# Kernel tuning notes

Measured on AMD Instinct MI355X. Metric: run time of the kernel, lower is better.

Reference implementation:

```python
import jax, jax.numpy as jnp
import numpy as np

N_HEAD, D_MODEL, D_K, D_V = 16, 1024, 64, 64
BIAS_WEIGHT = 1.0
NEG = -10000.0


def setup_inputs() -> dict:
    key = jax.random.key(0)
    ks = jax.random.split(key, 9)
    B, L = 2, 2048
    q = jax.random.normal(ks[0], (B, L, D_MODEL), dtype=jnp.float32)
    k = jax.random.normal(ks[1], (B, L, D_MODEL), dtype=jnp.float32)
    v = jax.random.normal(ks[2], (B, L, D_MODEL), dtype=jnp.float32)
    mask = jax.random.randint(ks[3], (B, L, L), 0, 2, dtype=jnp.int32)
    bias = jax.random.normal(ks[4], (B, L, L), dtype=jnp.float32)
    s = 1.0 / np.sqrt(D_MODEL)
    w_qs = jax.random.uniform(ks[5], (D_MODEL, N_HEAD * D_K), jnp.float32, -s, s)
    w_ks = jax.random.uniform(ks[6], (D_MODEL, N_HEAD * D_K), jnp.float32, -s, s)
    w_vs = jax.random.uniform(ks[7], (D_MODEL, N_HEAD * D_V), jnp.float32, -s, s)
    w_fc = jax.random.uniform(ks[8], (N_HEAD * D_V, D_MODEL), jnp.float32, -s, s)
    return {"q": q, "k": k, "v": v, "mask": mask, "bias": bias,
            "w_qs": w_qs, "w_ks": w_ks, "w_vs": w_vs, "w_fc": w_fc}


def reference(q, k, v, mask, bias, w_qs, w_ks, w_vs, w_fc):
    B, Lq, _ = q.shape
    # project and split heads: [B, H, L, d]
    qh = (q @ w_qs).reshape(B, Lq, N_HEAD, D_K).transpose(0, 2, 1, 3)
    kh = (k @ w_ks).reshape(B, k.shape[1], N_HEAD, D_K).transpose(0, 2, 1, 3)
    vh = (v @ w_vs).reshape(B, v.shape[1], N_HEAD, D_V).transpose(0, 2, 1, 3)
    temperature = D_K ** 0.5
    attn = jnp.einsum('bhqd,bhkd->bhqk', qh / temperature, kh)
    attn = attn + bias[:, None, :, :] * BIAS_WEIGHT
    attn = jnp.where(mask[:, None, :, :] == 0, NEG, attn)
    attn = jax.nn.softmax(attn, axis=-1)
    out = jnp.einsum('bhqk,bhkd->bhqd', attn, vh)
    out = out.transpose(0, 2, 1, 3).reshape(B, Lq, N_HEAD * D_V)
    return out @ w_fc
```

## Files before the change

### kernel.cpp

```cpp
#include <hip/hip_runtime.h>
#include <cstddef>

#define DEV static __device__ __forceinline__

typedef float f32x4 __attribute__((ext_vector_type(4)));
typedef __bf16 bf16x8 __attribute__((ext_vector_type(8)));
typedef __bf16 bf16x4v __attribute__((ext_vector_type(4)));
typedef unsigned short u16x8 __attribute__((ext_vector_type(8)));
typedef unsigned short u16x4 __attribute__((ext_vector_type(4)));
typedef unsigned u32x2 __attribute__((ext_vector_type(2)));
typedef unsigned u32x4 __attribute__((ext_vector_type(4)));
typedef _Float16 f16;
typedef _Float16 f16x4 __attribute__((ext_vector_type(4)));

constexpr int BB = 2, LL = 2048, DM = 1024, NH = 16, DK = 64;
constexpr float LOG2E = 1.44269504f;

DEV unsigned short f2bf(float f) {
  unsigned u = __builtin_bit_cast(unsigned, f);
  u += 0x7fffu + ((u >> 16) & 1u);
  return (unsigned short)(u >> 16);
}
DEV u16x4 cvt4(f32x4 v) {
  bf16x4v b = __builtin_convertvector(v, bf16x4v);
  return __builtin_bit_cast(u16x4, b);
}
DEV bf16x8 asbf(u16x8 v) { return __builtin_bit_cast(bf16x8, v); }
DEV f32x4 mfma16(u16x8 a, u16x8 b, f32x4 c) {
  return __builtin_amdgcn_mfma_f32_16x16x32_bf16(asbf(a), asbf(b), c, 0, 0, 0);
}
#if __has_builtin(__builtin_amdgcn_exp2f)
DEV float fexp2(float x) { return __builtin_amdgcn_exp2f(x); }
#else
DEV float fexp2(float x) { return exp2f(x); }
#endif
DEV void swap32(unsigned& a, unsigned& b) {
#if __has_builtin(__builtin_amdgcn_permlane32_swap)
  u32x2 r = __builtin_amdgcn_permlane32_swap(a, b, false, false);
  a = r[0]; b = r[1];
#else
  asm("v_permlane32_swap_b32 %0, %1" : "+v"(a), "+v"(b));
#endif
}
DEV void swap16(unsigned& a, unsigned& b) {
#if __has_builtin(__builtin_amdgcn_permlane16_swap)
  u32x2 r = __builtin_amdgcn_permlane16_swap(a, b, false, false);
  a = r[0]; b = r[1];
#else
  asm("v_permlane16_swap_b32 %0, %1" : "+v"(a), "+v"(b));
#endif
}
DEV void g2lds16(const void* g, void* l) {
  __builtin_amdgcn_global_load_lds(
      (const __attribute__((address_space(1))) unsigned int*)g,
      (__attribute__((address_space(3))) unsigned int*)l, 16, 0, 0);
}

__global__ __launch_bounds__(256) void prep_all(
    const float* __restrict__ w0, const float* __restrict__ w1,
    const float* __restrict__ w2, const float* __restrict__ w3,
    unsigned short* __restrict__ wT, const int* __restrict__ mask,
    const float* __restrict__ bias, f16* __restrict__ bmf,
    const float* __restrict__ s0, const float* __restrict__ s1,
    const float* __restrict__ s2, unsigned short* __restrict__ qkvb) {
  int f = blockIdx.x, t = threadIdx.x;
  if (f < 4096) {
    __shared__ float tile[32][33];
    int z = f >> 10, rem = f & 1023;
    int k0 = (rem >> 5) * 32, n0 = (rem & 31) * 32;
    const float* W = (z == 0) ? w0 : (z == 1) ? w1 : (z == 2) ? w2 : w3;
    unsigned short* out = wT + (size_t)z * DM * DM;
    int tx = t & 31, ty = t >> 5;
#pragma unroll
    for (int p = 0; p < 4; p++)
      tile[ty + 8 * p][tx] = W[(size_t)(k0 + ty + 8 * p) * DM + n0 + tx];
    __syncthreads();
#pragma unroll
    for (int p = 0; p < 4; p++)
      out[(size_t)(n0 + ty + 8 * p) * DM + k0 + tx] = f2bf(tile[tx][ty + 8 * p]);
  } else if (f < 12288) {
    int f2 = f - 4096;
    int w = t >> 6, lane = t & 63;
    int bq = f2 >> 5;
    int kt = (f2 & 31) * 4 + w;
    int b = bq >> 7, qt = bq & 127;
    int q = qt * 16 + (lane & 15);
    int k = kt * 16 + (lane >> 4) * 4;
    size_t src = ((size_t)b * LL + q) * LL + k;
    int4 mk = *(const int4*)(mask + src);
    float4 bs = *(const float4*)(bias + src);
    f16x4 o;
    o[0] = (f16)((mk.x == 0 ? -10000.f : bs.x) * LOG2E);
    o[1] = (f16)((mk.y == 0 ? -10000.f : bs.y) * LOG2E);
    o[2] = (f16)((mk.z == 0 ? -10000.f : bs.z) * LOG2E);
    o[3] = (f16)((mk.w == 0 ? -10000.f : bs.w) * LOG2E);
    *(f16x4*)(bmf + ((size_t)bq * 128 + kt) * 256 + lane * 4) = o;
  } else {
    int f3 = f - 12288;
    int z = f3 >> 11;
    const float* src = (z == 0) ? s0 : (z == 1) ? s1 : s2;
    size_t i = ((size_t)(f3 & 2047) * 256 + t) * 8;
    float4 a = *(const float4*)(src + i);
    float4 b = *(const float4*)(src + i + 4);
    u16x8 o;
    o[0] = f2bf(a.x); o[1] = f2bf(a.y); o[2] = f2bf(a.z); o[3] = f2bf(a.w);
    o[4] = f2bf(b.x); o[5] = f2bf(b.y); o[6] = f2bf(b.z); o[7] = f2bf(b.w);
    *(u16x8*)(qkvb + (size_t)z * (size_t)(BB * LL) * DM + i) = o;
  }
}

template <int KITERS>
DEV void gemm_core(const unsigned short* __restrict__ A,
                   const unsigned short* __restrict__ BT,
                   unsigned short* Al, unsigned short* Bl,
                   int m0, int n0, int k0beg, int t, f32x4 (&acc)[4][4]) {
  int lane = t & 63, c = lane & 15, qd = lane >> 4;
  int w = t >> 6, wm = w >> 1, wn = w & 1;
  int r0 = t >> 3;
  int gsw = (t & 7) ^ (r0 & 7);

#pragma unroll 1
  for (int kk = 0; kk < KITERS; ++kk) {
    int k0 = k0beg + kk * 64;
#pragma unroll
    for (int p = 0; p < 4; ++p) {
      g2lds16(&A[(size_t)(m0 + 32 * p + r0) * DM + k0 + 8 * gsw],
              &Al[p * 2048 + w * 512]);
      g2lds16(&BT[(size_t)(n0 + 32 * p + r0) * DM + k0 + 8 * gsw],
              &Bl[p * 2048 + w * 512]);
    }
    __syncthreads();
#pragma unroll
    for (int ks = 0; ks < 2; ++ks) {
      u16x8 af[4], bfr[4];
#pragma unroll
      for (int mt = 0; mt < 4; ++mt)
        af[mt] = *(const u16x8*)&Al[(64 * wm + 16 * mt + c) * 64 +
                                    (((4 * ks + qd) ^ (c & 7)) << 3)];
#pragma unroll
      for (int nt = 0; nt < 4; ++nt)
        bfr[nt] = *(const u16x8*)&Bl[(64 * wn + 16 * nt + c) * 64 +
                                     (((4 * ks + qd) ^ (c & 7)) << 3)];
#pragma unroll
      for (int mt = 0; mt < 4; ++mt)
#pragma unroll
        for (int nt = 0; nt < 4; ++nt)
          acc[mt][nt] = mfma16(af[mt], bfr[nt], acc[mt][nt]);
    }
    __syncthreads();
  }
}

__global__ __launch_bounds__(256, 3) void proj_gemm(
    const unsigned short* __restrict__ qkvb, const unsigned short* __restrict__ wT,
    unsigned short* __restrict__ qh, unsigned short* __restrict__ kh,
    unsigned short* __restrict__ vT) {
  __shared__ unsigned short Al[128 * 64];
  __shared__ unsigned short Bl[128 * 64];
  int o = blockIdx.x;
  int wg = (o & 7) * 96 + (o >> 3);
  int z = wg >> 8, rem = wg & 255;
  int m0 = (rem >> 3) * 128, n0 = (rem & 7) * 128;
  const unsigned short* A = qkvb + (size_t)z * BB * LL * DM;
  const unsigned short* BT = wT + (size_t)z * DM * DM;
  int t = threadIdx.x, lane = t & 63, c = lane & 15, qd = lane >> 4;
  int w = t >> 6, wm = w >> 1, wn = w & 1;
  f32x4 acc[4][4] = {};
  gemm_core<DM / 64>(A, BT, Al, Bl, m0, n0, 0, t, acc);

  if (z == 2) {
#pragma unroll
    for (int mt = 0; mt < 4; ++mt)
#pragma unroll
      for (int nt = 0; nt < 4; ++nt) {
        int n = n0 + 64 * wn + 16 * nt + c;
        int h = n >> 6, d = n & 63;
        int m = m0 + 64 * wm + 16 * mt + 4 * qd;
        int b = m >> 11, l = m & 2047;
        *(u16x4*)&vT[(((size_t)b * NH + h) * DK + d) * LL + l] = cvt4(acc[mt][nt]);
      }
  } else {
    unsigned short* Ch = z ? kh : qh;
    float scale = z ? 1.0f : 0.125f * LOG2E;
#pragma unroll
    for (int mt = 0; mt < 4; ++mt)
#pragma unroll
      for (int nt = 0; nt < 4; ++nt) {
        int n = n0 + 64 * wn + 16 * nt + c;
        int h = n >> 6, d = n & 63;
#pragma unroll
        for (int i = 0; i < 4; ++i) {
          int m = m0 + 64 * wm + 16 * mt + 4 * qd + i;
          int b = m >> 11, l = m & 2047;
          Ch[(((size_t)b * NH + h) * LL + l) * DK + d] = f2bf(acc[mt][nt][i] * scale);
        }
      }
  }
}

__global__ __launch_bounds__(256, 3) void fc_gemm(const unsigned short* __restrict__ A,
                                                  const unsigned short* __restrict__ BT,
                                                  float* __restrict__ C) {
  __shared__ unsigned short Al[128 * 64];
  __shared__ unsigned short Bl[128 * 64];
  int o = blockIdx.x;
  int wg = (o & 7) * 32 + (o >> 3);
  int m0 = (wg >> 3) * 128, n0 = (wg & 7) * 128;
  int t = threadIdx.x, lane = t & 63, c = lane & 15, qd = lane >> 4;
  int w = t >> 6, wm = w >> 1, wn = w & 1;
  f32x4 acc[4][4] = {};
  gemm_core<DM / 64>(A, BT, Al, Bl, m0, n0, 0, t, acc);
#pragma unroll
  for (int mt = 0; mt < 4; ++mt)
#pragma unroll
    for (int nt = 0; nt < 4; ++nt) {
      int n = n0 + 64 * wn + 16 * nt + c;
#pragma unroll
      for (int i = 0; i < 4; ++i) {
        int m = m0 + 64 * wm + 16 * mt + 4 * qd + i;
        C[(size_t)m * DM + n] = acc[mt][nt][i];
      }
    }
}

__global__ __launch_bounds__(256, 4) void attn_kern(
    const unsigned short* __restrict__ qh, const unsigned short* __restrict__ kh,
    const unsigned short* __restrict__ vT, const f16* __restrict__ bmf,
    unsigned short* __restrict__ O) {
  __shared__ unsigned short Kb[2][4096];
  __shared__ unsigned short Vb[2][4096];

  int t = threadIdx.x, w = t >> 6, lane = t & 63, c = lane & 15, qd = lane >> 4;
  int q0 = blockIdx.x * 64, h = blockIdx.y, b = blockIdx.z;
  const unsigned short* Q = qh + (((size_t)b * NH + h) * LL + q0) * DK;
  const unsigned short* K = kh + ((size_t)b * NH + h) * LL * DK;
  const unsigned short* V = vT + ((size_t)b * NH + h) * DK * LL;
  const f16* BMF = bmf + (((size_t)b * 128 + blockIdx.x * 4 + w) * 128) * 256 +
                   lane * 4;
  int rt = t >> 3, gg = t & 7;

#pragma unroll
  for (int r = 0; r < 2; ++r) {
    int row = r * 32 + rt;
    int sc = ((gg ^ (row & 7)) << 3);
    g2lds16(&Q[(size_t)row * DK + sc], &Kb[1][r * 2048 + w * 512]);
    g2lds16(&K[(size_t)row * DK + sc], &Kb[0][r * 2048 + w * 512]);
    g2lds16(&V[(size_t)row * LL + sc], &Vb[0][r * 2048 + w * 512]);
  }
  f16x4 bA[4], bB[4];
#pragma unroll
  for (int mt = 0; mt < 4; ++mt) bA[mt] = *(const f16x4*)&BMF[(size_t)mt * 256];
  __syncthreads();

  u16x8 qf[2];
#pragma unroll
  for (int ks = 0; ks < 2; ++ks)
    qf[ks] = *(const u16x8*)&Kb[1][(16 * w + c) * 64 +
                                   (((4 * ks + qd) ^ (c & 7)) << 3)];
  __syncthreads();

  const u16x8 ones = {0x3F80, 0x3F80, 0x3F80, 0x3F80,
                      0x3F80, 0x3F80, 0x3F80, 0x3F80};
  f32x4 lacc = {};
  f32x4 oacc[4] = {};

  auto body = [&](int it, f16x4 (&bc)[4], f16x4 (&bn)[4]) {
    int cur = it & 1;
    const unsigned short* Kl = Kb[cur];
    const unsigned short* Vt = Vb[cur];
    if (it + 1 < 32) {
      int nb = cur ^ 1, kt1 = (it + 1) * 64;
#pragma unroll
      for (int r = 0; r < 2; ++r) {
        int row = r * 32 + rt;
        int sc = ((gg ^ (row & 7)) << 3);
        g2lds16(&K[(size_t)(kt1 + row) * DK + sc], &Kb[nb][r * 2048 + w * 512]);
        g2lds16(&V[(size_t)row * LL + kt1 + sc], &Vb[nb][r * 2048 + w * 512]);
      }
#pragma unroll
      for (int mt = 0; mt < 4; ++mt)
        bn[mt] = *(const f16x4*)&BMF[(size_t)((it + 1) * 4 + mt) * 256];
    }

    f32x4 s[4];
    __builtin_amdgcn_s_setprio(1);
#pragma unroll
    for (int mt = 0; mt < 4; ++mt) {
      int row = 16 * mt + c;
      u16x8 k0f = *(const u16x8*)&Kl[row * 64 + ((qd ^ (c & 7)) << 3)];
      u16x8 k1f = *(const u16x8*)&Kl[row * 64 + (((4 + qd) ^ (c & 7)) << 3)];
      f16x4 b4 = bc[mt];
      f32x4 z = {(float)b4[0], (float)b4[1], (float)b4[2], (float)b4[3]};
      z = mfma16(k0f, qf[0], z);
      s[mt] = mfma16(k1f, qf[1], z);
    }
    __builtin_amdgcn_s_setprio(0);
    u16x8 pf[2];
    {
      unsigned L[4], H[4];
#pragma unroll
      for (int mt = 0; mt < 4; ++mt) {
        f32x4 p;
#pragma unroll
        for (int i = 0; i < 4; ++i) p[i] = fexp2(s[mt][i]);
        u32x2 lw = __builtin_bit_cast(u32x2, cvt4(p));
        L[mt] = lw[0];
        H[mt] = lw[1];
      }
#pragma unroll
      for (int ks = 0; ks < 2; ++ks) {
        unsigned l0 = L[2 * ks], l1 = L[2 * ks + 1];
        unsigned h0 = H[2 * ks], h1 = H[2 * ks + 1];
        swap32(l0, l1); swap16(l0, l1);
        swap32(h0, h1); swap16(h0, h1);
        u32x4 pw = {l0, h0, l1, h1};
        pf[ks] = __builtin_bit_cast(u16x8, pw);
      }
    }
    __builtin_amdgcn_s_setprio(1);
    lacc = mfma16(ones, pf[0], lacc);
    lacc = mfma16(ones, pf[1], lacc);
#pragma unroll
    for (int dt = 0; dt < 4; ++dt) {
      int row = 16 * dt + c;
      u16x8 v0f = *(const u16x8*)&Vt[row * 64 + ((qd ^ (c & 7)) << 3)];
      u16x8 v1f = *(const u16x8*)&Vt[row * 64 + (((4 + qd) ^ (c & 7)) << 3)];
      oacc[dt] = mfma16(v0f, pf[0], oacc[dt]);
      oacc[dt] = mfma16(v1f, pf[1], oacc[dt]);
    }
    __builtin_amdgcn_s_setprio(0);
    __syncthreads();
  };

#pragma unroll 1
  for (int it = 0; it < 32; it += 2) {
    body(it, bA, bB);
    body(it + 1, bB, bA);
  }

  {
    float rl = 1.f / lacc[0];
    size_t orow = ((size_t)b * LL + q0 + 16 * w + c) * DM + h * DK;
#pragma unroll
    for (int dt = 0; dt < 4; ++dt)
      *(u16x4*)&O[orow + 16 * dt + 4 * qd] = cvt4(oacc[dt] * rl);
  }
}

extern "C" void kernel_launch(void* const* d_in, const int* in_sizes, int n_in,
                              void* d_out, int out_size, void* d_ws, size_t ws_size,
                              hipStream_t stream) {
  (void)in_sizes; (void)n_in; (void)ws_size; (void)out_size;
  const float* q = (const float*)d_in[0];
  const float* k = (const float*)d_in[1];
  const float* v = (const float*)d_in[2];
  const int* mask = (const int*)d_in[3];
  const float* bias = (const float*)d_in[4];
  const float* w_qs = (const float*)d_in[5];
  const float* w_ks = (const float*)d_in[6];
  const float* w_vs = (const float*)d_in[7];
  const float* w_fc = (const float*)d_in[8];

  char* ws = (char*)d_ws;
  const size_t MB = 1024 * 1024;
  unsigned short* wT = (unsigned short*)(ws);
  f16* bmf = (f16*)(ws + 8 * MB);
  unsigned short* qkvb = (unsigned short*)(ws + 24 * MB);
  unsigned short* qh = (unsigned short*)(ws + 48 * MB);
  unsigned short* kh = (unsigned short*)(ws + 56 * MB);
  unsigned short* vhT = (unsigned short*)(ws + 64 * MB);
  unsigned short* Obuf = (unsigned short*)(ws + 72 * MB);

  prep_all<<<dim3(18432), dim3(256), 0, stream>>>(w_qs, w_ks, w_vs, w_fc, wT,
                                                  mask, bias, bmf, q, k, v, qkvb);
  proj_gemm<<<dim3(768), 256, 0, stream>>>(qkvb, wT, qh, kh, vhT);
  attn_kern<<<dim3(32, 16, 2), 256, 0, stream>>>(qh, kh, vhT, bmf, Obuf);
  fc_gemm<<<dim3(256), 256, 0, stream>>>(Obuf, wT + (size_t)3 * DM * DM,
                                         (float*)d_out);
}
```

Baseline: 267.5 us.

## Use two-wave attention blocks with each wave handling 32 query rows

The attention kernel moves from 4 waves of 16 query rows each to 2 waves of 32 query rows each. Each K/V fragment read from LDS now feeds twice as many MFMAs, cutting LDS read traffic per unit of work. The launch is flattened to a 1D grid with a block-index swizzle that groups nearby work onto the same XCD, which should improve L2 reuse of K/V. The costs are more registers per wave (doubled accumulators and bias buffers), fewer waves per block to hide latency, and a lower launch-bounds occupancy hint.

Result: no change. 270.9 us (+1.2%).

```diff
diff --git a/kernel.cpp b/kernel.cpp
--- a/kernel.cpp
+++ b/kernel.cpp
@@ -223,7 +223,7 @@
     }
 }
 
-__global__ __launch_bounds__(256, 4) void attn_kern(
+__global__ __launch_bounds__(128, 2) void attn_kern(
     const unsigned short* __restrict__ qh, const unsigned short* __restrict__ kh,
     const unsigned short* __restrict__ vT, const f16* __restrict__ bmf,
     unsigned short* __restrict__ O) {
@@ -231,78 +231,93 @@
   __shared__ unsigned short Vb[2][4096];
 
   int t = threadIdx.x, w = t >> 6, lane = t & 63, c = lane & 15, qd = lane >> 4;
-  int q0 = blockIdx.x * 64, h = blockIdx.y, b = blockIdx.z;
+  int o = blockIdx.x;
+  int wg = (o & 7) * 128 + (o >> 3);
+  int x = wg & 31, h = (wg >> 5) & 15, b = wg >> 9;
+  int q0 = x * 64;
   const unsigned short* Q = qh + (((size_t)b * NH + h) * LL + q0) * DK;
   const unsigned short* K = kh + ((size_t)b * NH + h) * LL * DK;
   const unsigned short* V = vT + ((size_t)b * NH + h) * DK * LL;
-  const f16* BMF = bmf + (((size_t)b * 128 + blockIdx.x * 4 + w) * 128) * 256 +
-                   lane * 4;
+  const f16* BMF0 = bmf + (((size_t)b * 128 + x * 4 + 2 * w) * 128) * 256 + lane * 4;
+  const f16* BMF1 = BMF0 + (size_t)128 * 256;
   int rt = t >> 3, gg = t & 7;
 
 #pragma unroll
-  for (int r = 0; r < 2; ++r) {
-    int row = r * 32 + rt;
+  for (int r = 0; r < 4; ++r) {
+    int row = r * 16 + rt;
     int sc = ((gg ^ (row & 7)) << 3);
-    g2lds16(&Q[(size_t)row * DK + sc], &Kb[1][r * 2048 + w * 512]);
-    g2lds16(&K[(size_t)row * DK + sc], &Kb[0][r * 2048 + w * 512]);
-    g2lds16(&V[(size_t)row * LL + sc], &Vb[0][r * 2048 + w * 512]);
-  }
-  f16x4 bA[4], bB[4];
-#pragma unroll
-  for (int mt = 0; mt < 4; ++mt) bA[mt] = *(const f16x4*)&BMF[(size_t)mt * 256];
+    g2lds16(&Q[(size_t)row * DK + sc], &Kb[1][r * 1024 + w * 512]);
+    g2lds16(&K[(size_t)row * DK + sc], &Kb[0][r * 1024 + w * 512]);
+    g2lds16(&V[(size_t)row * LL + sc], &Vb[0][r * 1024 + w * 512]);
+  }
+  f16x4 bA[8], bB[8];
+#pragma unroll
+  for (int nt = 0; nt < 2; ++nt)
+#pragma unroll
+    for (int mt = 0; mt < 4; ++mt)
+      bA[nt * 4 + mt] = *(const f16x4*)((nt ? BMF1 : BMF0) + (size_t)mt * 256);
   __syncthreads();
 
-  u16x8 qf[2];
-#pragma unroll
-  for (int ks = 0; ks < 2; ++ks)
-    qf[ks] = *(const u16x8*)&Kb[1][(16 * w + c) * 64 +
-                                   (((4 * ks + qd) ^ (c & 7)) << 3)];
+  u16x8 qf[2][2];
+#pragma unroll
+  for (int nt = 0; nt < 2; ++nt)
+#pragma unroll
+    for (int ks = 0; ks < 2; ++ks)
+      qf[nt][ks] = *(const u16x8*)&Kb[1][(32 * w + 16 * nt + c) * 64 +
+                                         (((4 * ks + qd) ^ (c & 7)) << 3)];
   __syncthreads();
 
   const u16x8 ones = {0x3F80, 0x3F80, 0x3F80, 0x3F80,
                       0x3F80, 0x3F80, 0x3F80, 0x3F80};
-  f32x4 lacc = {};
-  f32x4 oacc[4] = {};
-
-  auto body = [&](int it, f16x4 (&bc)[4], f16x4 (&bn)[4]) {
+  f32x4 lacc[2] = {};
+  f32x4 oacc[4][2] = {};
+
+  auto body = [&](int it, f16x4 (&bc)[8], f16x4 (&bn)[8]) {
     int cur = it & 1;
     const unsigned short* Kl = Kb[cur];
     const unsigned short* Vt = Vb[cur];
     if (it + 1 < 32) {
       int nb = cur ^ 1, kt1 = (it + 1) * 64;
 #pragma unroll
-      for (int r = 0; r < 2; ++r) {
-        int row = r * 32 + rt;
+      for (int r = 0; r < 4; ++r) {
+        int row = r * 16 + rt;
         int sc = ((gg ^ (row & 7)) << 3);
-        g2lds16(&K[(size_t)(kt1 + row) * DK + sc], &Kb[nb][r * 2048 + w * 512]);
-        g2lds16(&V[(size_t)row * LL + kt1 + sc], &Vb[nb][r * 2048 + w * 512]);
-      }
-#pragma unroll
-      for (int mt = 0; mt < 4; ++mt)
-        bn[mt] = *(const f16x4*)&BMF[(size_t)((it + 1) * 4 + mt) * 256];
-    }
-
-    f32x4 s[4];
+        g2lds16(&K[(size_t)(kt1 + row) * DK + sc], &Kb[nb][r * 1024 + w * 512]);
+        g2lds16(&V[(size_t)row * LL + kt1 + sc], &Vb[nb][r * 1024 + w * 512]);
+      }
+#pragma unroll
+      for (int nt = 0; nt < 2; ++nt)
+#pragma unroll
+        for (int mt = 0; mt < 4; ++mt)
+          bn[nt * 4 + mt] = *(const f16x4*)((nt ? BMF1 : BMF0) +
+                                            (size_t)((it + 1) * 4 + mt) * 256);
+    }
+
+    f32x4 s[4][2];
     __builtin_amdgcn_s_setprio(1);
 #pragma unroll
     for (int mt = 0; mt < 4; ++mt) {
       int row = 16 * mt + c;
       u16x8 k0f = *(const u16x8*)&Kl[row * 64 + ((qd ^ (c & 7)) << 3)];
       u16x8 k1f = *(const u16x8*)&Kl[row * 64 + (((4 + qd) ^ (c & 7)) << 3)];
-      f16x4 b4 = bc[mt];
-      f32x4 z = {(float)b4[0], (float)b4[1], (float)b4[2], (float)b4[3]};
-      z = mfma16(k0f, qf[0], z);
-      s[mt] = mfma16(k1f, qf[1], z);
+#pragma unroll
+      for (int nt = 0; nt < 2; ++nt) {
+        f16x4 b4 = bc[nt * 4 + mt];
+        f32x4 z = {(float)b4[0], (float)b4[1], (float)b4[2], (float)b4[3]};
+        z = mfma16(k0f, qf[nt][0], z);
+        s[mt][nt] = mfma16(k1f, qf[nt][1], z);
+      }
     }
     __builtin_amdgcn_s_setprio(0);
-    u16x8 pf[2];
-    {
+    u16x8 pf[2][2];
+#pragma unroll
+    for (int nt = 0; nt < 2; ++nt) {
       unsigned L[4], H[4];
 #pragma unroll
       for (int mt = 0; mt < 4; ++mt) {
         f32x4 p;
 #pragma unroll
-        for (int i = 0; i < 4; ++i) p[i] = fexp2(s[mt][i]);
+        for (int i = 0; i < 4; ++i) p[i] = fexp2(s[mt][nt][i]);
         u32x2 lw = __builtin_bit_cast(u32x2, cvt4(p));
         L[mt] = lw[0];
         H[mt] = lw[1];
@@ -314,19 +329,25 @@
         swap32(l0, l1); swap16(l0, l1);
         swap32(h0, h1); swap16(h0, h1);
         u32x4 pw = {l0, h0, l1, h1};
-        pf[ks] = __builtin_bit_cast(u16x8, pw);
+        pf[nt][ks] = __builtin_bit_cast(u16x8, pw);
       }
     }
     __builtin_amdgcn_s_setprio(1);
-    lacc = mfma16(ones, pf[0], lacc);
-    lacc = mfma16(ones, pf[1], lacc);
+#pragma unroll
+    for (int nt = 0; nt < 2; ++nt) {
+      lacc[nt] = mfma16(ones, pf[nt][0], lacc[nt]);
+      lacc[nt] = mfma16(ones, pf[nt][1], lacc[nt]);
+    }
 #pragma unroll
     for (int dt = 0; dt < 4; ++dt) {
       int row = 16 * dt + c;
       u16x8 v0f = *(const u16x8*)&Vt[row * 64 + ((qd ^ (c & 7)) << 3)];
       u16x8 v1f = *(const u16x8*)&Vt[row * 64 + (((4 + qd) ^ (c & 7)) << 3)];
-      oacc[dt] = mfma16(v0f, pf[0], oacc[dt]);
-      oacc[dt] = mfma16(v1f, pf[1], oacc[dt]);
+#pragma unroll
+      for (int nt = 0; nt < 2; ++nt) {
+        oacc[dt][nt] = mfma16(v0f, pf[nt][0], oacc[dt][nt]);
+        oacc[dt][nt] = mfma16(v1f, pf[nt][1], oacc[dt][nt]);
+      }
     }
     __builtin_amdgcn_s_setprio(0);
     __syncthreads();
@@ -338,12 +359,13 @@
     body(it + 1, bB, bA);
   }
 
-  {
-    float rl = 1.f / lacc[0];
-    size_t orow = ((size_t)b * LL + q0 + 16 * w + c) * DM + h * DK;
+#pragma unroll
+  for (int nt = 0; nt < 2; ++nt) {
+    float rl = 1.f / lacc[nt][0];
+    size_t orow = ((size_t)b * LL + q0 + 32 * w + 16 * nt + c) * DM + h * DK;
 #pragma unroll
     for (int dt = 0; dt < 4; ++dt)
-      *(u16x4*)&O[orow + 16 * dt + 4 * qd] = cvt4(oacc[dt] * rl);
+      *(u16x4*)&O[orow + 16 * dt + 4 * qd] = cvt4(oacc[dt][nt] * rl);
   }
 }
 
@@ -374,7 +396,7 @@
   prep_all<<<dim3(18432), dim3(256), 0, stream>>>(w_qs, w_ks, w_vs, w_fc, wT,
                                                   mask, bias, bmf, q, k, v, qkvb);
   proj_gemm<<<dim3(768), 256, 0, stream>>>(qkvb, wT, qh, kh, vhT);
-  attn_kern<<<dim3(32, 16, 2), 256, 0, stream>>>(qh, kh, vhT, bmf, Obuf);
+  attn_kern<<<dim3(1024), dim3(128), 0, stream>>>(qh, kh, vhT, bmf, Obuf);
   fc_gemm<<<dim3(256), 256, 0, stream>>>(Obuf, wT + (size_t)3 * DM * DM,
                                          (float*)d_out);
 }
```

## Double-buffer fc_gemm LDS tiles and remap attention blocks across XCDs

Applied to the files above, without the earlier changes.

The output projection GEMM replaces the shared gemm_core call with an inline double-buffered loop that prefetches the next K-tile into a second LDS buffer while MFMAs run on the current one. This hides global-to-LDS latency at the cost of doubling LDS use and lowering the occupancy hint from 3 to 2 blocks per CU. The attention kernel switches to a 1D grid with a swizzled block index, so that consecutive blocks on the same XCD share a head's K/V and bias data for better L2 reuse.

Result: slower. 276.3 us (+3.3%).

```diff
diff --git a/kernel.cpp b/kernel.cpp
--- a/kernel.cpp
+++ b/kernel.cpp
@@ -198,18 +198,58 @@
   }
 }
 
-__global__ __launch_bounds__(256, 3) void fc_gemm(const unsigned short* __restrict__ A,
+__global__ __launch_bounds__(256, 2) void fc_gemm(const unsigned short* __restrict__ A,
                                                   const unsigned short* __restrict__ BT,
                                                   float* __restrict__ C) {
-  __shared__ unsigned short Al[128 * 64];
-  __shared__ unsigned short Bl[128 * 64];
+  __shared__ unsigned short Al[2][128 * 64];
+  __shared__ unsigned short Bl[2][128 * 64];
   int o = blockIdx.x;
   int wg = (o & 7) * 32 + (o >> 3);
   int m0 = (wg >> 3) * 128, n0 = (wg & 7) * 128;
   int t = threadIdx.x, lane = t & 63, c = lane & 15, qd = lane >> 4;
   int w = t >> 6, wm = w >> 1, wn = w & 1;
+  int r0 = t >> 3, gsw = (t & 7) ^ (r0 & 7);
   f32x4 acc[4][4] = {};
-  gemm_core<DM / 64>(A, BT, Al, Bl, m0, n0, 0, t, acc);
+
+  auto stage = [&](int kk, int buf) {
+    int k0 = kk * 64;
+#pragma unroll
+    for (int p = 0; p < 4; ++p) {
+      g2lds16(&A[(size_t)(m0 + 32 * p + r0) * DM + k0 + 8 * gsw],
+              &Al[buf][p * 2048 + w * 512]);
+      g2lds16(&BT[(size_t)(n0 + 32 * p + r0) * DM + k0 + 8 * gsw],
+              &Bl[buf][p * 2048 + w * 512]);
+    }
+  };
+  auto compute = [&](int buf) {
+#pragma unroll
+    for (int ks = 0; ks < 2; ++ks) {
+      u16x8 af[4], bfr[4];
+#pragma unroll
+      for (int mt = 0; mt < 4; ++mt)
+        af[mt] = *(const u16x8*)&Al[buf][(64 * wm + 16 * mt + c) * 64 +
+                                         (((4 * ks + qd) ^ (c & 7)) << 3)];
+#pragma unroll
+      for (int nt = 0; nt < 4; ++nt)
+        bfr[nt] = *(const u16x8*)&Bl[buf][(64 * wn + 16 * nt + c) * 64 +
+                                          (((4 * ks + qd) ^ (c & 7)) << 3)];
+#pragma unroll
+      for (int mt = 0; mt < 4; ++mt)
+#pragma unroll
+        for (int nt = 0; nt < 4; ++nt)
+          acc[mt][nt] = mfma16(af[mt], bfr[nt], acc[mt][nt]);
+    }
+  };
+
+  stage(0, 0);
+  __syncthreads();
+#pragma unroll 1
+  for (int kk = 0; kk < 16; ++kk) {
+    if (kk + 1 < 16) stage(kk + 1, (kk + 1) & 1);
+    compute(kk & 1);
+    __syncthreads();
+  }
+
 #pragma unroll
   for (int mt = 0; mt < 4; ++mt)
 #pragma unroll
@@ -231,12 +271,14 @@
   __shared__ unsigned short Vb[2][4096];
 
   int t = threadIdx.x, w = t >> 6, lane = t & 63, c = lane & 15, qd = lane >> 4;
-  int q0 = blockIdx.x * 64, h = blockIdx.y, b = blockIdx.z;
+  int o = blockIdx.x;
+  int wg = (o & 7) * 128 + (o >> 3);
+  int x = wg & 31, h = (wg >> 5) & 15, b = wg >> 9;
+  int q0 = x * 64;
   const unsigned short* Q = qh + (((size_t)b * NH + h) * LL + q0) * DK;
   const unsigned short* K = kh + ((size_t)b * NH + h) * LL * DK;
   const unsigned short* V = vT + ((size_t)b * NH + h) * DK * LL;
-  const f16* BMF = bmf + (((size_t)b * 128 + blockIdx.x * 4 + w) * 128) * 256 +
-                   lane * 4;
+  const f16* BMF = bmf + (((size_t)b * 128 + x * 4 + w) * 128) * 256 + lane * 4;
   int rt = t >> 3, gg = t & 7;
 
 #pragma unroll
@@ -374,7 +416,7 @@
   prep_all<<<dim3(18432), dim3(256), 0, stream>>>(w_qs, w_ks, w_vs, w_fc, wT,
                                                   mask, bias, bmf, q, k, v, qkvb);
   proj_gemm<<<dim3(768), 256, 0, stream>>>(qkvb, wT, qh, kh, vhT);
-  attn_kern<<<dim3(32, 16, 2), 256, 0, stream>>>(qh, kh, vhT, bmf, Obuf);
+  attn_kern<<<dim3(1024), dim3(256), 0, stream>>>(qh, kh, vhT, bmf, Obuf);
   fc_gemm<<<dim3(256), 256, 0, stream>>>(Obuf, wT + (size_t)3 * DM * DM,
                                          (float*)d_out);
 }
```

## Software-pipeline attention: overlap next QK^T MFMA with current softmax and PV

Applied to the files above, without the earlier changes.

Restructures the attention loop so the QK^T scores for the next key tile are computed while the current tile's exp/convert and PV MFMAs run, using a triple-buffered V in LDS and a prologue/epilogue. It also flattens the grid to 1D and remaps block indices so each group of 8 consecutive blocks is spread across different (batch, head, query) positions, aiming for better XCD/L2 locality. The intent is to hide MFMA and transcendental latency by interleaving them, at the cost of more LDS (an extra V buffer) and higher register pressure from keeping two score sets live.

New measurement: 267.1 us. No clear change (-0.1%).

```diff
diff --git a/kernel.cpp b/kernel.cpp
--- a/kernel.cpp
+++ b/kernel.cpp
@@ -228,17 +228,20 @@
     const unsigned short* __restrict__ vT, const f16* __restrict__ bmf,
     unsigned short* __restrict__ O) {
   __shared__ unsigned short Kb[2][4096];
-  __shared__ unsigned short Vb[2][4096];
+  __shared__ unsigned short Vb[3][4096];
 
   int t = threadIdx.x, w = t >> 6, lane = t & 63, c = lane & 15, qd = lane >> 4;
-  int q0 = blockIdx.x * 64, h = blockIdx.y, b = blockIdx.z;
+  int o = blockIdx.x;
+  int wg = (o & 7) * 128 + (o >> 3);
+  int x = wg & 31, h = (wg >> 5) & 15, b = wg >> 9;
+  int q0 = x * 64;
   const unsigned short* Q = qh + (((size_t)b * NH + h) * LL + q0) * DK;
   const unsigned short* K = kh + ((size_t)b * NH + h) * LL * DK;
   const unsigned short* V = vT + ((size_t)b * NH + h) * DK * LL;
-  const f16* BMF = bmf + (((size_t)b * 128 + blockIdx.x * 4 + w) * 128) * 256 +
-                   lane * 4;
+  const f16* BMF = bmf + (((size_t)b * 128 + x * 4 + w) * 128) * 256 + lane * 4;
   int rt = t >> 3, gg = t & 7;
 
+  f16x4 bc[4], bn[4];
 #pragma unroll
   for (int r = 0; r < 2; ++r) {
     int row = r * 32 + rt;
@@ -247,9 +250,8 @@
     g2lds16(&K[(size_t)row * DK + sc], &Kb[0][r * 2048 + w * 512]);
     g2lds16(&V[(size_t)row * LL + sc], &Vb[0][r * 2048 + w * 512]);
   }
-  f16x4 bA[4], bB[4];
-#pragma unroll
-  for (int mt = 0; mt < 4; ++mt) bA[mt] = *(const f16x4*)&BMF[(size_t)mt * 256];
+#pragma unroll
+  for (int mt = 0; mt < 4; ++mt) bc[mt] = *(const f16x4*)&BMF[(size_t)mt * 256];
   __syncthreads();
 
   u16x8 qf[2];
@@ -259,31 +261,85 @@
                                    (((4 * ks + qd) ^ (c & 7)) << 3)];
   __syncthreads();
 
+  {
+#pragma unroll
+    for (int r = 0; r < 2; ++r) {
+      int row = r * 32 + rt;
+      int sc = ((gg ^ (row & 7)) << 3);
+      g2lds16(&K[(size_t)(64 + row) * DK + sc], &Kb[1][r * 2048 + w * 512]);
+      g2lds16(&V[(size_t)row * LL + 64 + sc], &Vb[1][r * 2048 + w * 512]);
+    }
+#pragma unroll
+    for (int mt = 0; mt < 4; ++mt)
+      bn[mt] = *(const f16x4*)&BMF[(size_t)(4 + mt) * 256];
+  }
+  f32x4 sP[4];
+  __builtin_amdgcn_s_setprio(1);
+#pragma unroll
+  for (int mt = 0; mt < 4; ++mt) {
+    int row = 16 * mt + c;
+    u16x8 k0f = *(const u16x8*)&Kb[0][row * 64 + ((qd ^ (c & 7)) << 3)];
+    u16x8 k1f = *(const u16x8*)&Kb[0][row * 64 + (((4 + qd) ^ (c & 7)) << 3)];
+    f16x4 b4 = bc[mt];
+    f32x4 z = {(float)b4[0], (float)b4[1], (float)b4[2], (float)b4[3]};
+    z = mfma16(k0f, qf[0], z);
+    sP[mt] = mfma16(k1f, qf[1], z);
+  }
+  __builtin_amdgcn_s_setprio(0);
+#pragma unroll
+  for (int mt = 0; mt < 4; ++mt) bc[mt] = bn[mt];
+  __syncthreads();
+
   const u16x8 ones = {0x3F80, 0x3F80, 0x3F80, 0x3F80,
                       0x3F80, 0x3F80, 0x3F80, 0x3F80};
   f32x4 lacc = {};
   f32x4 oacc[4] = {};
-
-  auto body = [&](int it, f16x4 (&bc)[4], f16x4 (&bn)[4]) {
-    int cur = it & 1;
-    const unsigned short* Kl = Kb[cur];
-    const unsigned short* Vt = Vb[cur];
-    if (it + 1 < 32) {
-      int nb = cur ^ 1, kt1 = (it + 1) * 64;
+  unsigned short* Vr = Vb[0];
+  unsigned short* Vc = Vb[1];
+  unsigned short* Vw = Vb[2];
+
+#pragma unroll 1
+  for (int j = 1; j < 32; ++j) {
+    const unsigned short* Kl = Kb[j & 1];
+    unsigned short* Kw = Kb[(j + 1) & 1];
+    if (j + 1 < 32) {
+      int kt1 = (j + 1) * 64;
 #pragma unroll
       for (int r = 0; r < 2; ++r) {
         int row = r * 32 + rt;
         int sc = ((gg ^ (row & 7)) << 3);
-        g2lds16(&K[(size_t)(kt1 + row) * DK + sc], &Kb[nb][r * 2048 + w * 512]);
-        g2lds16(&V[(size_t)row * LL + kt1 + sc], &Vb[nb][r * 2048 + w * 512]);
+        g2lds16(&K[(size_t)(kt1 + row) * DK + sc], &Kw[r * 2048 + w * 512]);
+        g2lds16(&V[(size_t)row * LL + kt1 + sc], &Vw[r * 2048 + w * 512]);
       }
 #pragma unroll
       for (int mt = 0; mt < 4; ++mt)
-        bn[mt] = *(const f16x4*)&BMF[(size_t)((it + 1) * 4 + mt) * 256];
-    }
-
-    f32x4 s[4];
+        bn[mt] = *(const f16x4*)&BMF[(size_t)((j + 1) * 4 + mt) * 256];
+    }
+
     __builtin_amdgcn_s_setprio(1);
+    u16x8 pf[2];
+    {
+      unsigned L[4], H[4];
+#pragma unroll
+      for (int mt = 0; mt < 4; ++mt) {
+        f32x4 p;
+#pragma unroll
+        for (int i = 0; i < 4; ++i) p[i] = fexp2(sP[mt][i]);
+        u32x2 lw = __builtin_bit_cast(u32x2, cvt4(p));
+        L[mt] = lw[0];
+        H[mt] = lw[1];
+      }
+#pragma unroll
+      for (int ks = 0; ks < 2; ++ks) {
+        unsigned l0 = L[2 * ks], l1 = L[2 * ks + 1];
+        unsigned h0 = H[2 * ks], h1 = H[2 * ks + 1];
+        swap32(l0, l1); swap16(l0, l1);
+        swap32(h0, h1); swap16(h0, h1);
+        u32x4 pw = {l0, h0, l1, h1};
+        pf[ks] = __builtin_bit_cast(u16x8, pw);
+      }
+    }
+    f32x4 sN[4];
 #pragma unroll
     for (int mt = 0; mt < 4; ++mt) {
       int row = 16 * mt + c;
@@ -292,50 +348,56 @@
       f16x4 b4 = bc[mt];
       f32x4 z = {(float)b4[0], (float)b4[1], (float)b4[2], (float)b4[3]};
       z = mfma16(k0f, qf[0], z);
-      s[mt] = mfma16(k1f, qf[1], z);
-    }
-    __builtin_amdgcn_s_setprio(0);
-    u16x8 pf[2];
-    {
-      unsigned L[4], H[4];
-#pragma unroll
-      for (int mt = 0; mt < 4; ++mt) {
-        f32x4 p;
-#pragma unroll
-        for (int i = 0; i < 4; ++i) p[i] = fexp2(s[mt][i]);
-        u32x2 lw = __builtin_bit_cast(u32x2, cvt4(p));
-        L[mt] = lw[0];
-        H[mt] = lw[1];
-      }
-#pragma unroll
-      for (int ks = 0; ks < 2; ++ks) {
-        unsigned l0 = L[2 * ks], l1 = L[2 * ks + 1];
-        unsigned h0 = H[2 * ks], h1 = H[2 * ks + 1];
-        swap32(l0, l1); swap16(l0, l1);
-        swap32(h0, h1); swap16(h0, h1);
-        u32x4 pw = {l0, h0, l1, h1};
-        pf[ks] = __builtin_bit_cast(u16x8, pw);
-      }
-    }
-    __builtin_amdgcn_s_setprio(1);
+      sN[mt] = mfma16(k1f, qf[1], z);
+    }
     lacc = mfma16(ones, pf[0], lacc);
     lacc = mfma16(ones, pf[1], lacc);
 #pragma unroll
     for (int dt = 0; dt < 4; ++dt) {
       int row = 16 * dt + c;
-      u16x8 v0f = *(const u16x8*)&Vt[row * 64 + ((qd ^ (c & 7)) << 3)];
-      u16x8 v1f = *(const u16x8*)&Vt[row * 64 + (((4 + qd) ^ (c & 7)) << 3)];
+      u16x8 v0f = *(const u16x8*)&Vr[row * 64 + ((qd ^ (c & 7)) << 3)];
+      u16x8 v1f = *(const u16x8*)&Vr[row * 64 + (((4 + qd) ^ (c & 7)) << 3)];
       oacc[dt] = mfma16(v0f, pf[0], oacc[dt]);
       oacc[dt] = mfma16(v1f, pf[1], oacc[dt]);
     }
     __builtin_amdgcn_s_setprio(0);
+
+#pragma unroll
+    for (int mt = 0; mt < 4; ++mt) { sP[mt] = sN[mt]; bc[mt] = bn[mt]; }
+    unsigned short* tv = Vr; Vr = Vc; Vc = Vw; Vw = tv;
     __syncthreads();
-  };
-
-#pragma unroll 1
-  for (int it = 0; it < 32; it += 2) {
-    body(it, bA, bB);
-    body(it + 1, bB, bA);
+  }
+
+  {
+    u16x8 pf[2];
+    unsigned L[4], H[4];
+#pragma unroll
+    for (int mt = 0; mt < 4; ++mt) {
+      f32x4 p;
+#pragma unroll
+      for (int i = 0; i < 4; ++i) p[i] = fexp2(sP[mt][i]);
+      u32x2 lw = __builtin_bit_cast(u32x2, cvt4(p));
+      L[mt] = lw[0]; H[mt] = lw[1];
+    }
+#pragma unroll
+    for (int ks = 0; ks < 2; ++ks) {
+      unsigned l0 = L[2 * ks], l1 = L[2 * ks + 1];
+      unsigned h0 = H[2 * ks], h1 = H[2 * ks + 1];
+      swap32(l0, l1); swap16(l0, l1);
+      swap32(h0, h1); swap16(h0, h1);
+      u32x4 pw = {l0, h0, l1, h1};
+      pf[ks] = __builtin_bit_cast(u16x8, pw);
+    }
+    lacc = mfma16(ones, pf[0], lacc);
+    lacc = mfma16(ones, pf[1], lacc);
+#pragma unroll
+    for (int dt = 0; dt < 4; ++dt) {
+      int row = 16 * dt + c;
+      u16x8 v0f = *(const u16x8*)&Vr[row * 64 + ((qd ^ (c & 7)) << 3)];
+      u16x8 v1f = *(const u16x8*)&Vr[row * 64 + (((4 + qd) ^ (c & 7)) << 3)];
+      oacc[dt] = mfma16(v0f, pf[0], oacc[dt]);
+      oacc[dt] = mfma16(v1f, pf[1], oacc[dt]);
+    }
   }
 
   {
@@ -374,7 +436,7 @@
   prep_all<<<dim3(18432), dim3(256), 0, stream>>>(w_qs, w_ks, w_vs, w_fc, wT,
                                                   mask, bias, bmf, q, k, v, qkvb);
   proj_gemm<<<dim3(768), 256, 0, stream>>>(qkvb, wT, qh, kh, vhT);
-  attn_kern<<<dim3(32, 16, 2), 256, 0, stream>>>(qh, kh, vhT, bmf, Obuf);
+  attn_kern<<<dim3(1024), dim3(256), 0, stream>>>(qh, kh, vhT, bmf, Obuf);
   fc_gemm<<<dim3(256), 256, 0, stream>>>(Obuf, wT + (size_t)3 * DM * DM,
                                          (float*)d_out);
 }
```
